# Kernel tuning notes

Measured on AMD Instinct MI355X. Metric: run time of the kernel, lower is better.

The kernel has to match this reference:

```python
import jax, jax.numpy as jnp
import numpy as np

N = 100000
E = 3200000
F_IN = 128
HID = 64
NUM_GRAPHS = 512
NUM_CLASSES = 2


def setup_inputs() -> dict:
    key = jax.random.key(0)
    ks = jax.random.split(key, 8)
    x = jax.random.normal(ks[0], (N, F_IN), dtype=jnp.float32)
    edge_index = jax.random.randint(ks[1], (2, E), 0, N, dtype=jnp.int64)
    batch = jnp.sort(jax.random.randint(ks[2], (N,), 0, NUM_GRAPHS, dtype=jnp.int64))
    # Glorot-style init for GCN weights, PyTorch default-style for fc
    W1 = jax.random.normal(ks[3], (F_IN, HID), dtype=jnp.float32) * (1.0 / np.sqrt(F_IN))
    b1 = jnp.zeros((HID,), dtype=jnp.float32)
    W2 = jax.random.normal(ks[4], (HID, HID), dtype=jnp.float32) * (1.0 / np.sqrt(HID))
    b2 = jnp.zeros((HID,), dtype=jnp.float32)
    Wfc = jax.random.normal(ks[5], (HID, NUM_CLASSES), dtype=jnp.float32) * (1.0 / np.sqrt(HID))
    bfc = jax.random.normal(ks[6], (NUM_CLASSES,), dtype=jnp.float32) * 0.01
    return {"x": x, "edge_index": edge_index, "batch": batch,
            "W1": W1, "b1": b1, "W2": W2, "b2": b2, "Wfc": Wfc, "bfc": bfc}


def _gcn_conv(x, row, col, deg_inv_sqrt, W, b):
    """PyG GCNConv: out[col] += d^{-1/2}[row] d^{-1/2}[col] * (x W)[row], self-loops included in row/col."""
    h = x @ W  # [N, out_dim]
    norm = deg_inv_sqrt[row] * deg_inv_sqrt[col]  # [E+N]
    msgs = h[row] * norm[:, None]  # gather + scale
    out = jax.ops.segment_sum(msgs, col, num_segments=N)  # scatter-add
    return out + b


def reference(x, edge_index, batch, W1, b1, W2, b2, Wfc, bfc):
    # add self-loops once (shared normalization for both layers)
    loop = jnp.arange(N, dtype=edge_index.dtype)
    row = jnp.concatenate([edge_index[0], loop])  # sources
    col = jnp.concatenate([edge_index[1], loop])  # targets
    deg = jax.ops.segment_sum(jnp.ones_like(col, dtype=x.dtype), col, num_segments=N)
    deg_inv_sqrt = jnp.where(deg > 0, jax.lax.rsqrt(deg), 0.0)

    h = jax.nn.relu(_gcn_conv(x, row, col, deg_inv_sqrt, W1, b1))
    h = jax.nn.relu(_gcn_conv(h, row, col, deg_inv_sqrt, W2, b2))

    # global_mean_pool over batch ids
    sums = jax.ops.segment_sum(h, batch, num_segments=NUM_GRAPHS)  # [G, HID]
    counts = jax.ops.segment_sum(jnp.ones((N,), dtype=h.dtype), batch, num_segments=NUM_GRAPHS)
    pooled = sums / jnp.maximum(counts, 1.0)[:, None]

    # dropout p=0.5 is identity in eval mode
    return pooled @ Wfc + bfc  # [G, NUM_CLASSES]
```

## Files before the change

### kernel.cpp

```cpp
#include <hip/hip_runtime.h>

#define N_NODES   100000
#define N_EDGES   3200000
#define F_INP     128
#define HID       64
#define N_GRAPHS  512
#define N_CLASSES 2
#define NB        782
#define SCAT_BLOCKS 256
#define CHUNK     (N_EDGES / SCAT_BLOCKS)

__device__ __forceinline__ unsigned short f2bf(float f) {
    unsigned int u = __float_as_uint(f);
    return (unsigned short)((u + 0x7FFFu + ((u >> 16) & 1u)) >> 16);
}
__device__ __forceinline__ float bf_lo(unsigned int u) { return __uint_as_float(u << 16); }
__device__ __forceinline__ float bf_hi(unsigned int u) { return __uint_as_float(u & 0xFFFF0000u); }

__global__ __launch_bounds__(256) void hist_kernel(const int* __restrict__ ei,
                                                   int* __restrict__ bcnt,
                                                   int* __restrict__ bh) {
    __shared__ int hist[NB];
    for (int i = threadIdx.x; i < NB; i += 256) hist[i] = 0;
    __syncthreads();
    const int e0 = blockIdx.x * CHUNK, e1 = e0 + CHUNK;
    for (int e = e0 + threadIdx.x; e < e1; e += 256)
        atomicAdd(&hist[ei[N_EDGES + e] >> 7], 1);
    __syncthreads();
    for (int i = threadIdx.x; i < NB; i += 256) {
        int v = hist[i];
        bh[(size_t)blockIdx.x * NB + i] = v;
        if (v) atomicAdd(&bcnt[i], v);
    }
}

__global__ __launch_bounds__(1024) void scan_kernel(const int* __restrict__ bcnt,
                                                    int* __restrict__ boff) {
    __shared__ int s[1024];
    const int tid = threadIdx.x;
    const int v = (tid < NB) ? bcnt[tid] : 0;
    s[tid] = v;
    __syncthreads();
    for (int d = 1; d < 1024; d <<= 1) {
        int t = (tid >= d) ? s[tid - d] : 0;
        __syncthreads();
        s[tid] += t;
        __syncthreads();
    }
    if (tid <= NB) boff[tid] = s[tid] - v;
}

__global__ __launch_bounds__(256) void bbase_kernel(int* __restrict__ bh,
                                                    const int* __restrict__ boff) {
    __shared__ int s[256];
    const int b = blockIdx.x;
    const int tid = threadIdx.x;
    const int v = bh[(size_t)tid * NB + b];
    s[tid] = v;
    __syncthreads();
    for (int d = 1; d < 256; d <<= 1) {
        int t = (tid >= d) ? s[tid - d] : 0;
        __syncthreads();
        s[tid] += t;
        __syncthreads();
    }
    bh[(size_t)tid * NB + b] = boff[b] + s[tid] - v;
}

__global__ __launch_bounds__(256) void scatter_kernel(const int* __restrict__ ei,
                                                      const int* __restrict__ bh,
                                                      int* __restrict__ pairs) {
    __shared__ int lbase[NB];
    __shared__ int lcur[NB];
    for (int i = threadIdx.x; i < NB; i += 256) {
        lbase[i] = bh[(size_t)blockIdx.x * NB + i];
        lcur[i] = 0;
    }
    __syncthreads();
    const int e0 = blockIdx.x * CHUNK, e1 = e0 + CHUNK;
    for (int e = e0 + threadIdx.x; e < e1; e += 256) {
        int c = ei[N_EDGES + e];
        int r = ei[e];
        int b = c >> 7;
        int off = atomicAdd(&lcur[b], 1);
        pairs[lbase[b] + off] = r | ((c & 127) << 17);
    }
}

__global__ __launch_bounds__(256) void csr_kernel(const int* __restrict__ pairs,
                                                  const int* __restrict__ boff,
                                                  int* __restrict__ adj,
                                                  int* __restrict__ offs,
                                                  float* __restrict__ dis) {
    __shared__ int cnt[128];
    __shared__ int sc[128];
    __shared__ int base[128];
    __shared__ int cur[128];
    const int tid = threadIdx.x;
    const int b = blockIdx.x;
    const int beg = boff[b], end = boff[b + 1];
    if (tid < 128) { cnt[tid] = 0; cur[tid] = 0; }
    __syncthreads();
    for (int e = beg + tid; e < end; e += 256)
        atomicAdd(&cnt[pairs[e] >> 17], 1);
    __syncthreads();
    if (tid < 128) sc[tid] = cnt[tid];
    __syncthreads();
    for (int d = 1; d < 128; d <<= 1) {
        int t = (tid >= d && tid < 128) ? sc[tid - d] : 0;
        __syncthreads();
        if (tid < 128) sc[tid] += t;
        __syncthreads();
    }
    if (tid < 128) base[tid] = beg + sc[tid] - cnt[tid];
    __syncthreads();
    for (int e = beg + tid; e < end; e += 256) {
        int v = pairs[e];
        int lc = v >> 17;
        int o = atomicAdd(&cur[lc], 1);
        adj[base[lc] + o] = v & 131071;
    }
    const int n = (b << 7) + tid;
    if (tid < 128 && n < N_NODES) {
        offs[n] = base[tid];
        dis[n] = rsqrtf((float)cnt[tid] + 1.0f);
    }
    if (b == 0 && tid == 0) offs[N_NODES] = N_EDGES;
}

__global__ void counts_kernel(const int* __restrict__ batch, int* __restrict__ counts) {
    const int g = blockIdx.x * blockDim.x + threadIdx.x;
    if (g >= N_GRAPHS) return;
    int lo = 0, hi = N_NODES;
    while (lo < hi) { int m = (lo + hi) >> 1; if (batch[m] < g) lo = m + 1; else hi = m; }
    const int l0 = lo;
    lo = 0; hi = N_NODES;
    while (lo < hi) { int m = (lo + hi) >> 1; if (batch[m] < g + 1) lo = m + 1; else hi = m; }
    counts[g] = lo - l0;
}

__global__ __launch_bounds__(256) void mm1_kernel(const float* __restrict__ x,
                                                  const float* __restrict__ W1,
                                                  const float* __restrict__ dis,
                                                  unsigned short* __restrict__ p) {
    __shared__ float ws[F_INP * HID];
    for (int i = threadIdx.x; i < F_INP * HID / 4; i += 256)
        ((float4*)ws)[i] = ((const float4*)W1)[i];
    __syncthreads();
    const int tx = threadIdx.x & 15;
    const int ty = threadIdx.x >> 4;
    const int row0 = blockIdx.x * 64 + ty * 4;
    int r[4];
#pragma unroll
    for (int i = 0; i < 4; ++i) r[i] = min(row0 + i, N_NODES - 1);
    float acc[4][4] = {};
#pragma unroll 2
    for (int k = 0; k < F_INP; k += 4) {
        float4 a[4];
#pragma unroll
        for (int i = 0; i < 4; ++i)
            a[i] = *(const float4*)(x + (size_t)r[i] * F_INP + k);
        float4 w0 = *(const float4*)(ws + (k + 0) * HID + tx * 4);
        float4 w1 = *(const float4*)(ws + (k + 1) * HID + tx * 4);
        float4 w2 = *(const float4*)(ws + (k + 2) * HID + tx * 4);
        float4 w3 = *(const float4*)(ws + (k + 3) * HID + tx * 4);
#pragma unroll
        for (int i = 0; i < 4; ++i) {
            acc[i][0] += a[i].x * w0.x + a[i].y * w1.x + a[i].z * w2.x + a[i].w * w3.x;
            acc[i][1] += a[i].x * w0.y + a[i].y * w1.y + a[i].z * w2.y + a[i].w * w3.y;
            acc[i][2] += a[i].x * w0.z + a[i].y * w1.z + a[i].z * w2.z + a[i].w * w3.z;
            acc[i][3] += a[i].x * w0.w + a[i].y * w1.w + a[i].z * w2.w + a[i].w * w3.w;
        }
    }
#pragma unroll
    for (int i = 0; i < 4; ++i) {
        int rr = row0 + i;
        if (rr < N_NODES) {
            float d = dis[rr];
            ushort4 o;
            o.x = f2bf(d * acc[i][0]);
            o.y = f2bf(d * acc[i][1]);
            o.z = f2bf(d * acc[i][2]);
            o.w = f2bf(d * acc[i][3]);
            *(ushort4*)(p + (size_t)rr * HID + tx * 4) = o;
        }
    }
}

__global__ __launch_bounds__(256) void mm2_kernel(const unsigned short* __restrict__ hb,
                                                  const float* __restrict__ W2,
                                                  const float* __restrict__ dis,
                                                  unsigned short* __restrict__ p) {
    __shared__ float ws[HID * HID];
    for (int i = threadIdx.x; i < HID * HID / 4; i += 256)
        ((float4*)ws)[i] = ((const float4*)W2)[i];
    __syncthreads();
    const int tx = threadIdx.x & 15;
    const int ty = threadIdx.x >> 4;
    const int row0 = blockIdx.x * 64 + ty * 4;
    int r[4];
#pragma unroll
    for (int i = 0; i < 4; ++i) r[i] = min(row0 + i, N_NODES - 1);
    float acc[4][4] = {};
#pragma unroll 2
    for (int k = 0; k < HID; k += 8) {
        uint4 a[4];
#pragma unroll
        for (int i = 0; i < 4; ++i)
            a[i] = *(const uint4*)(hb + (size_t)r[i] * HID + k);
        float4 w[8];
#pragma unroll
        for (int m = 0; m < 8; ++m)
            w[m] = *(const float4*)(ws + (k + m) * HID + tx * 4);
#pragma unroll
        for (int i = 0; i < 4; ++i) {
            float h0 = bf_lo(a[i].x), h1 = bf_hi(a[i].x);
            float h2 = bf_lo(a[i].y), h3 = bf_hi(a[i].y);
            float h4 = bf_lo(a[i].z), h5 = bf_hi(a[i].z);
            float h6 = bf_lo(a[i].w), h7 = bf_hi(a[i].w);
            acc[i][0] += h0 * w[0].x + h1 * w[1].x + h2 * w[2].x + h3 * w[3].x
                       + h4 * w[4].x + h5 * w[5].x + h6 * w[6].x + h7 * w[7].x;
            acc[i][1] += h0 * w[0].y + h1 * w[1].y + h2 * w[2].y + h3 * w[3].y
                       + h4 * w[4].y + h5 * w[5].y + h6 * w[6].y + h7 * w[7].y;
            acc[i][2] += h0 * w[0].z + h1 * w[1].z + h2 * w[2].z + h3 * w[3].z
                       + h4 * w[4].z + h5 * w[5].z + h6 * w[6].z + h7 * w[7].z;
            acc[i][3] += h0 * w[0].w + h1 * w[1].w + h2 * w[2].w + h3 * w[3].w
                       + h4 * w[4].w + h5 * w[5].w + h6 * w[6].w + h7 * w[7].w;
        }
    }
#pragma unroll
    for (int i = 0; i < 4; ++i) {
        int rr = row0 + i;
        if (rr < N_NODES) {
            float d = dis[rr];
            ushort4 o;
            o.x = f2bf(d * acc[i][0]);
            o.y = f2bf(d * acc[i][1]);
            o.z = f2bf(d * acc[i][2]);
            o.w = f2bf(d * acc[i][3]);
            *(ushort4*)(p + (size_t)rr * HID + tx * 4) = o;
        }
    }
}

__device__ __forceinline__ float gather_node(const unsigned short* __restrict__ p,
                                             const int* __restrict__ adj,
                                             int c, int beg, int end, int q, int g) {
    float acc[8];
    {
        uint4 s = *(const uint4*)(p + (size_t)c * HID + g * 8);
        float sm = (q == 0) ? 1.f : 0.f;
        acc[0] = sm * bf_lo(s.x); acc[1] = sm * bf_hi(s.x);
        acc[2] = sm * bf_lo(s.y); acc[3] = sm * bf_hi(s.y);
        acc[4] = sm * bf_lo(s.z); acc[5] = sm * bf_hi(s.z);
        acc[6] = sm * bf_lo(s.w); acc[7] = sm * bf_hi(s.w);
    }
    int e = beg;
    for (; e + 32 <= end; e += 32) {
        int r0 = adj[e + q];
        int r1 = adj[e + 8 + q];
        int r2 = adj[e + 16 + q];
        int r3 = adj[e + 24 + q];
        uint4 v0 = *(const uint4*)(p + (size_t)r0 * HID + g * 8);
        uint4 v1 = *(const uint4*)(p + (size_t)r1 * HID + g * 8);
        uint4 v2 = *(const uint4*)(p + (size_t)r2 * HID + g * 8);
        uint4 v3 = *(const uint4*)(p + (size_t)r3 * HID + g * 8);
        acc[0] += (bf_lo(v0.x) + bf_lo(v1.x)) + (bf_lo(v2.x) + bf_lo(v3.x));
        acc[1] += (bf_hi(v0.x) + bf_hi(v1.x)) + (bf_hi(v2.x) + bf_hi(v3.x));
        acc[2] += (bf_lo(v0.y) + bf_lo(v1.y)) + (bf_lo(v2.y) + bf_lo(v3.y));
        acc[3] += (bf_hi(v0.y) + bf_hi(v1.y)) + (bf_hi(v2.y) + bf_hi(v3.y));
        acc[4] += (bf_lo(v0.z) + bf_lo(v1.z)) + (bf_lo(v2.z) + bf_lo(v3.z));
        acc[5] += (bf_hi(v0.z) + bf_hi(v1.z)) + (bf_hi(v2.z) + bf_hi(v3.z));
        acc[6] += (bf_lo(v0.w) + bf_lo(v1.w)) + (bf_lo(v2.w) + bf_lo(v3.w));
        acc[7] += (bf_hi(v0.w) + bf_hi(v1.w)) + (bf_hi(v2.w) + bf_hi(v3.w));
    }
    for (; e + 16 <= end; e += 16) {
        int r0 = adj[e + q];
        int r1 = adj[e + 8 + q];
        uint4 v0 = *(const uint4*)(p + (size_t)r0 * HID + g * 8);
        uint4 v1 = *(const uint4*)(p + (size_t)r1 * HID + g * 8);
        acc[0] += bf_lo(v0.x) + bf_lo(v1.x); acc[1] += bf_hi(v0.x) + bf_hi(v1.x);
        acc[2] += bf_lo(v0.y) + bf_lo(v1.y); acc[3] += bf_hi(v0.y) + bf_hi(v1.y);
        acc[4] += bf_lo(v0.z) + bf_lo(v1.z); acc[5] += bf_hi(v0.z) + bf_hi(v1.z);
        acc[6] += bf_lo(v0.w) + bf_lo(v1.w); acc[7] += bf_hi(v0.w) + bf_hi(v1.w);
    }
    for (; e < end; e += 8) {
        int idx = e + q;
        int r = adj[min(idx, end - 1)];
        float m = (idx < end) ? 1.f : 0.f;
        uint4 v = *(const uint4*)(p + (size_t)r * HID + g * 8);
        acc[0] = fmaf(m, bf_lo(v.x), acc[0]); acc[1] = fmaf(m, bf_hi(v.x), acc[1]);
        acc[2] = fmaf(m, bf_lo(v.y), acc[2]); acc[3] = fmaf(m, bf_hi(v.y), acc[3]);
        acc[4] = fmaf(m, bf_lo(v.z), acc[4]); acc[5] = fmaf(m, bf_hi(v.z), acc[5]);
        acc[6] = fmaf(m, bf_lo(v.w), acc[6]); acc[7] = fmaf(m, bf_hi(v.w), acc[7]);
    }
#pragma unroll
    for (int j = 0; j < 8; ++j) {
        acc[j] += __shfl_xor(acc[j], 8, 64);
        acc[j] += __shfl_xor(acc[j], 16, 64);
        acc[j] += __shfl_xor(acc[j], 32, 64);
    }
    return (q & 4) ? ((q & 2) ? ((q & 1) ? acc[7] : acc[6]) : ((q & 1) ? acc[5] : acc[4]))
                   : ((q & 2) ? ((q & 1) ? acc[3] : acc[2]) : ((q & 1) ? acc[1] : acc[0]));
}

__global__ __launch_bounds__(256) void gather1_kernel(const unsigned short* __restrict__ p,
                                                      const int* __restrict__ adj,
                                                      const int* __restrict__ offs,
                                                      const float* __restrict__ dis,
                                                      const float* __restrict__ b1,
                                                      unsigned short* __restrict__ hb) {
    const int lane = threadIdx.x & 63;
    const int q = lane >> 3, g = lane & 7;
    const int gwave = (blockIdx.x * blockDim.x + threadIdx.x) >> 6;
    const int nwaves = (gridDim.x * blockDim.x) >> 6;
    const float bj = b1[g * 8 + q];
    for (int c = gwave; c < N_NODES; c += nwaves) {
        const int beg = offs[c], end = offs[c + 1];
        float val = gather_node(p, adj, c, beg, end, q, g);
        hb[(size_t)c * HID + g * 8 + q] = f2bf(fmaxf(dis[c] * val + bj, 0.f));
    }
}

__global__ __launch_bounds__(256) void gather2_kernel(const unsigned short* __restrict__ p,
                                                      const int* __restrict__ adj,
                                                      const int* __restrict__ offs,
                                                      const float* __restrict__ dis,
                                                      const float* __restrict__ b2,
                                                      const int* __restrict__ batch,
                                                      float* __restrict__ sums) {
    const int lane = threadIdx.x & 63;
    const int q = lane >> 3, g = lane & 7;
    const int gwave = (blockIdx.x * blockDim.x + threadIdx.x) >> 6;
    const int nwaves = (gridDim.x * blockDim.x) >> 6;
    const float bj = b2[g * 8 + q];
    for (int c = gwave; c < N_NODES; c += nwaves) {
        const int beg = offs[c], end = offs[c + 1];
        float val = gather_node(p, adj, c, beg, end, q, g);
        float v = fmaxf(dis[c] * val + bj, 0.f);
        atomicAdd(&sums[(size_t)batch[c] * HID + g * 8 + q], v);
    }
}

__global__ void fc_kernel(const float* __restrict__ sums, const int* __restrict__ counts,
                          const float* __restrict__ Wfc, const float* __restrict__ bfc,
                          float* __restrict__ out) {
    const int g = blockIdx.x;
    const int j = threadIdx.x;
    float cnt = fmaxf((float)counts[g], 1.0f);
    float pj = sums[(size_t)g * HID + j] / cnt;
    float a0 = pj * Wfc[j * N_CLASSES + 0];
    float a1 = pj * Wfc[j * N_CLASSES + 1];
    for (int off = 32; off > 0; off >>= 1) {
        a0 += __shfl_down(a0, off, 64);
        a1 += __shfl_down(a1, off, 64);
    }
    if (j == 0) {
        out[g * N_CLASSES + 0] = a0 + bfc[0];
        out[g * N_CLASSES + 1] = a1 + bfc[1];
    }
}

extern "C" void kernel_launch(void* const* d_in, const int* in_sizes, int n_in,
                              void* d_out, int out_size, void* d_ws, size_t ws_size,
                              hipStream_t stream) {
    const float* x     = (const float*)d_in[0];
    const int*   ei    = (const int*)d_in[1];
    const int*   batch = (const int*)d_in[2];
    const float* W1    = (const float*)d_in[3];
    const float* b1    = (const float*)d_in[4];
    const float* W2    = (const float*)d_in[5];
    const float* b2    = (const float*)d_in[6];
    const float* Wfc   = (const float*)d_in[7];
    const float* bfc   = (const float*)d_in[8];
    float* out = (float*)d_out;

    char* ws = (char*)d_ws;
    size_t off = 0;
    auto alloc = [&](size_t bytes) -> void* {
        void* pp = ws + off;
        off += (bytes + 255) & ~(size_t)255;
        return pp;
    };
    int*   bcnt   = (int*)alloc((size_t)NB * 4);
    int*   boff   = (int*)alloc((size_t)(NB + 1) * 4);
    int*   bh     = (int*)alloc((size_t)SCAT_BLOCKS * NB * 4);
    float* dis    = (float*)alloc((size_t)N_NODES * 4);
    int*   pairs  = (int*)alloc((size_t)N_EDGES * 4);
    int*   adj    = (int*)alloc((size_t)N_EDGES * 4);
    int*   offs   = (int*)alloc((size_t)(N_NODES + 1) * 4);
    unsigned short* p  = (unsigned short*)alloc((size_t)N_NODES * HID * 2);
    unsigned short* hb = (unsigned short*)alloc((size_t)N_NODES * HID * 2);
    float* sums   = (float*)alloc((size_t)N_GRAPHS * HID * 4);
    int*   counts = (int*)alloc((size_t)N_GRAPHS * 4);

    hipMemsetAsync(bcnt, 0, (size_t)NB * 4, stream);
    hipMemsetAsync(sums, 0, (size_t)N_GRAPHS * HID * 4, stream);

    hist_kernel<<<SCAT_BLOCKS, 256, 0, stream>>>(ei, bcnt, bh);
    scan_kernel<<<1, 1024, 0, stream>>>(bcnt, boff);
    bbase_kernel<<<NB, 256, 0, stream>>>(bh, boff);
    scatter_kernel<<<SCAT_BLOCKS, 256, 0, stream>>>(ei, bh, pairs);
    csr_kernel<<<NB, 256, 0, stream>>>(pairs, boff, adj, offs, dis);
    counts_kernel<<<2, 256, 0, stream>>>(batch, counts);
    mm1_kernel<<<(N_NODES + 63) / 64, 256, 0, stream>>>(x, W1, dis, p);
    gather1_kernel<<<2048, 256, 0, stream>>>(p, adj, offs, dis, b1, hb);
    mm2_kernel<<<(N_NODES + 63) / 64, 256, 0, stream>>>(hb, W2, dis, p);
    gather2_kernel<<<2048, 256, 0, stream>>>(p, adj, offs, dis, b2, batch, sums);
    fc_kernel<<<N_GRAPHS, 64, 0, stream>>>(sums, counts, Wfc, bfc, out);
}
```

Before: 388.0 us.

## Stage GEMM tiles in LDS, segment-reduce pooling atomics, simplify prefix and reductions

Several independent changes. The per-bucket base computation becomes a serial per-thread scan in a small kernel. Both dense GEMMs first stage their 64-row input tile into shared memory with coalesced loads. The gather reduction uses a butterfly transpose-reduce with fewer shuffles. The gather loops switch to contiguous node ranges per wave so gather2 can accumulate per-graph partial sums and issue far fewer atomics. Graph counts move into the fc kernel via binary search, removing one launch. Extra shared memory in mm1 (64KB) may lower occupancy.

```diff
diff --git a/kernel.cpp b/kernel.cpp
--- a/kernel.cpp
+++ b/kernel.cpp
@@ -50,21 +50,18 @@
     if (tid <= NB) boff[tid] = s[tid] - v;
 }
 
-__global__ __launch_bounds__(256) void bbase_kernel(int* __restrict__ bh,
-                                                    const int* __restrict__ boff) {
-    __shared__ int s[256];
-    const int b = blockIdx.x;
-    const int tid = threadIdx.x;
-    const int v = bh[(size_t)tid * NB + b];
-    s[tid] = v;
-    __syncthreads();
-    for (int d = 1; d < 256; d <<= 1) {
-        int t = (tid >= d) ? s[tid - d] : 0;
-        __syncthreads();
-        s[tid] += t;
-        __syncthreads();
-    }
-    bh[(size_t)tid * NB + b] = boff[b] + s[tid] - v;
+__global__ __launch_bounds__(64) void bbase_kernel(int* __restrict__ bh,
+                                                   const int* __restrict__ boff) {
+    const int b = blockIdx.x * 64 + threadIdx.x;
+    if (b >= NB) return;
+    int base = boff[b];
+    for (int i = 0; i < SCAT_BLOCKS; i += 8) {
+        int v[8];
+#pragma unroll
+        for (int j = 0; j < 8; ++j) v[j] = bh[(size_t)(i + j) * NB + b];
+#pragma unroll
+        for (int j = 0; j < 8; ++j) { bh[(size_t)(i + j) * NB + b] = base; base += v[j]; }
+    }
 }
 
 __global__ __launch_bounds__(256) void scatter_kernel(const int* __restrict__ ei,
@@ -128,38 +125,32 @@
     if (b == 0 && tid == 0) offs[N_NODES] = N_EDGES;
 }
 
-__global__ void counts_kernel(const int* __restrict__ batch, int* __restrict__ counts) {
-    const int g = blockIdx.x * blockDim.x + threadIdx.x;
-    if (g >= N_GRAPHS) return;
-    int lo = 0, hi = N_NODES;
-    while (lo < hi) { int m = (lo + hi) >> 1; if (batch[m] < g) lo = m + 1; else hi = m; }
-    const int l0 = lo;
-    lo = 0; hi = N_NODES;
-    while (lo < hi) { int m = (lo + hi) >> 1; if (batch[m] < g + 1) lo = m + 1; else hi = m; }
-    counts[g] = lo - l0;
-}
-
 __global__ __launch_bounds__(256) void mm1_kernel(const float* __restrict__ x,
                                                   const float* __restrict__ W1,
                                                   const float* __restrict__ dis,
                                                   unsigned short* __restrict__ p) {
+    __shared__ float xs[64 * F_INP];
     __shared__ float ws[F_INP * HID];
     for (int i = threadIdx.x; i < F_INP * HID / 4; i += 256)
         ((float4*)ws)[i] = ((const float4*)W1)[i];
+    const long base4 = (long)blockIdx.x * (64 * F_INP / 4);
+    const long tot4 = (long)N_NODES * F_INP / 4;
+    for (int i = threadIdx.x; i < 64 * F_INP / 4; i += 256) {
+        float4 v = make_float4(0.f, 0.f, 0.f, 0.f);
+        if (base4 + i < tot4) v = ((const float4*)x)[base4 + i];
+        ((float4*)xs)[i] = v;
+    }
     __syncthreads();
     const int tx = threadIdx.x & 15;
     const int ty = threadIdx.x >> 4;
     const int row0 = blockIdx.x * 64 + ty * 4;
-    int r[4];
-#pragma unroll
-    for (int i = 0; i < 4; ++i) r[i] = min(row0 + i, N_NODES - 1);
     float acc[4][4] = {};
-#pragma unroll 2
+#pragma unroll 4
     for (int k = 0; k < F_INP; k += 4) {
         float4 a[4];
 #pragma unroll
         for (int i = 0; i < 4; ++i)
-            a[i] = *(const float4*)(x + (size_t)r[i] * F_INP + k);
+            a[i] = *(const float4*)(xs + (ty * 4 + i) * F_INP + k);
         float4 w0 = *(const float4*)(ws + (k + 0) * HID + tx * 4);
         float4 w1 = *(const float4*)(ws + (k + 1) * HID + tx * 4);
         float4 w2 = *(const float4*)(ws + (k + 2) * HID + tx * 4);
@@ -191,23 +182,28 @@
                                                   const float* __restrict__ W2,
                                                   const float* __restrict__ dis,
                                                   unsigned short* __restrict__ p) {
+    __shared__ unsigned short hs[64 * HID];
     __shared__ float ws[HID * HID];
     for (int i = threadIdx.x; i < HID * HID / 4; i += 256)
         ((float4*)ws)[i] = ((const float4*)W2)[i];
+    const long base8 = (long)blockIdx.x * (64 * HID / 8);
+    const long tot8 = (long)N_NODES * HID / 8;
+    for (int i = threadIdx.x; i < 64 * HID / 8; i += 256) {
+        uint4 v = make_uint4(0u, 0u, 0u, 0u);
+        if (base8 + i < tot8) v = ((const uint4*)hb)[base8 + i];
+        ((uint4*)hs)[i] = v;
+    }
     __syncthreads();
     const int tx = threadIdx.x & 15;
     const int ty = threadIdx.x >> 4;
     const int row0 = blockIdx.x * 64 + ty * 4;
-    int r[4];
-#pragma unroll
-    for (int i = 0; i < 4; ++i) r[i] = min(row0 + i, N_NODES - 1);
     float acc[4][4] = {};
 #pragma unroll 2
     for (int k = 0; k < HID; k += 8) {
         uint4 a[4];
 #pragma unroll
         for (int i = 0; i < 4; ++i)
-            a[i] = *(const uint4*)(hb + (size_t)r[i] * HID + k);
+            a[i] = *(const uint4*)(hs + (ty * 4 + i) * HID + k);
         float4 w[8];
 #pragma unroll
         for (int m = 0; m < 8; ++m)
@@ -294,14 +290,14 @@
         acc[4] = fmaf(m, bf_lo(v.z), acc[4]); acc[5] = fmaf(m, bf_hi(v.z), acc[5]);
         acc[6] = fmaf(m, bf_lo(v.w), acc[6]); acc[7] = fmaf(m, bf_hi(v.w), acc[7]);
     }
-#pragma unroll
-    for (int j = 0; j < 8; ++j) {
-        acc[j] += __shfl_xor(acc[j], 8, 64);
-        acc[j] += __shfl_xor(acc[j], 16, 64);
-        acc[j] += __shfl_xor(acc[j], 32, 64);
-    }
-    return (q & 4) ? ((q & 2) ? ((q & 1) ? acc[7] : acc[6]) : ((q & 1) ? acc[5] : acc[4]))
-                   : ((q & 2) ? ((q & 1) ? acc[3] : acc[2]) : ((q & 1) ? acc[1] : acc[0]));
+    const bool q0 = (q & 1) != 0, q1 = (q & 2) != 0, q2 = (q & 4) != 0;
+    float b0 = (q0 ? acc[1] : acc[0]) + __shfl_xor(q0 ? acc[0] : acc[1], 8, 64);
+    float b1 = (q0 ? acc[3] : acc[2]) + __shfl_xor(q0 ? acc[2] : acc[3], 8, 64);
+    float b2 = (q0 ? acc[5] : acc[4]) + __shfl_xor(q0 ? acc[4] : acc[5], 8, 64);
+    float b3 = (q0 ? acc[7] : acc[6]) + __shfl_xor(q0 ? acc[6] : acc[7], 8, 64);
+    float c0 = (q1 ? b1 : b0) + __shfl_xor(q1 ? b0 : b1, 16, 64);
+    float c1 = (q1 ? b3 : b2) + __shfl_xor(q1 ? b2 : b3, 16, 64);
+    return (q2 ? c1 : c0) + __shfl_xor(q2 ? c0 : c1, 32, 64);
 }
 
 __global__ __launch_bounds__(256) void gather1_kernel(const unsigned short* __restrict__ p,
@@ -314,8 +310,11 @@
     const int q = lane >> 3, g = lane & 7;
     const int gwave = (blockIdx.x * blockDim.x + threadIdx.x) >> 6;
     const int nwaves = (gridDim.x * blockDim.x) >> 6;
+    const int per = (N_NODES + nwaves - 1) / nwaves;
+    const int c0 = gwave * per;
+    const int c1 = min(N_NODES, c0 + per);
     const float bj = b1[g * 8 + q];
-    for (int c = gwave; c < N_NODES; c += nwaves) {
+    for (int c = c0; c < c1; ++c) {
         const int beg = offs[c], end = offs[c + 1];
         float val = gather_node(p, adj, c, beg, end, q, g);
         hb[(size_t)c * HID + g * 8 + q] = f2bf(fmaxf(dis[c] * val + bj, 0.f));
@@ -333,21 +332,39 @@
     const int q = lane >> 3, g = lane & 7;
     const int gwave = (blockIdx.x * blockDim.x + threadIdx.x) >> 6;
     const int nwaves = (gridDim.x * blockDim.x) >> 6;
+    const int per = (N_NODES + nwaves - 1) / nwaves;
+    const int c0 = gwave * per;
+    const int c1 = min(N_NODES, c0 + per);
     const float bj = b2[g * 8 + q];
-    for (int c = gwave; c < N_NODES; c += nwaves) {
+    const int feat = g * 8 + q;
+    float part = 0.f;
+    int gc = -1;
+    for (int c = c0; c < c1; ++c) {
         const int beg = offs[c], end = offs[c + 1];
         float val = gather_node(p, adj, c, beg, end, q, g);
         float v = fmaxf(dis[c] * val + bj, 0.f);
-        atomicAdd(&sums[(size_t)batch[c] * HID + g * 8 + q], v);
-    }
-}
-
-__global__ void fc_kernel(const float* __restrict__ sums, const int* __restrict__ counts,
+        int gid = batch[c];
+        if (gid != gc) {
+            if (gc >= 0) atomicAdd(&sums[(size_t)gc * HID + feat], part);
+            part = 0.f;
+            gc = gid;
+        }
+        part += v;
+    }
+    if (gc >= 0) atomicAdd(&sums[(size_t)gc * HID + feat], part);
+}
+
+__global__ void fc_kernel(const float* __restrict__ sums, const int* __restrict__ batch,
                           const float* __restrict__ Wfc, const float* __restrict__ bfc,
                           float* __restrict__ out) {
     const int g = blockIdx.x;
     const int j = threadIdx.x;
-    float cnt = fmaxf((float)counts[g], 1.0f);
+    int lo = 0, hi = N_NODES;
+    while (lo < hi) { int m = (lo + hi) >> 1; if (batch[m] < g) lo = m + 1; else hi = m; }
+    const int l0 = lo;
+    lo = 0; hi = N_NODES;
+    while (lo < hi) { int m = (lo + hi) >> 1; if (batch[m] < g + 1) lo = m + 1; else hi = m; }
+    float cnt = fmaxf((float)(lo - l0), 1.0f);
     float pj = sums[(size_t)g * HID + j] / cnt;
     float a0 = pj * Wfc[j * N_CLASSES + 0];
     float a1 = pj * Wfc[j * N_CLASSES + 1];
@@ -392,20 +409,18 @@
     unsigned short* p  = (unsigned short*)alloc((size_t)N_NODES * HID * 2);
     unsigned short* hb = (unsigned short*)alloc((size_t)N_NODES * HID * 2);
     float* sums   = (float*)alloc((size_t)N_GRAPHS * HID * 4);
-    int*   counts = (int*)alloc((size_t)N_GRAPHS * 4);
 
     hipMemsetAsync(bcnt, 0, (size_t)NB * 4, stream);
     hipMemsetAsync(sums, 0, (size_t)N_GRAPHS * HID * 4, stream);
 
     hist_kernel<<<SCAT_BLOCKS, 256, 0, stream>>>(ei, bcnt, bh);
     scan_kernel<<<1, 1024, 0, stream>>>(bcnt, boff);
-    bbase_kernel<<<NB, 256, 0, stream>>>(bh, boff);
+    bbase_kernel<<<(NB + 63) / 64, 64, 0, stream>>>(bh, boff);
     scatter_kernel<<<SCAT_BLOCKS, 256, 0, stream>>>(ei, bh, pairs);
     csr_kernel<<<NB, 256, 0, stream>>>(pairs, boff, adj, offs, dis);
-    counts_kernel<<<2, 256, 0, stream>>>(batch, counts);
     mm1_kernel<<<(N_NODES + 63) / 64, 256, 0, stream>>>(x, W1, dis, p);
     gather1_kernel<<<2048, 256, 0, stream>>>(p, adj, offs, dis, b1, hb);
     mm2_kernel<<<(N_NODES + 63) / 64, 256, 0, stream>>>(hb, W2, dis, p);
     gather2_kernel<<<2048, 256, 0, stream>>>(p, adj, offs, dis, b2, batch, sums);
-    fc_kernel<<<N_GRAPHS, 64, 0, stream>>>(sums, counts, Wfc, bfc, out);
-}
+    fc_kernel<<<N_GRAPHS, 64, 0, stream>>>(sums, batch, Wfc, bfc, out);
+}
```

Result: faster. 360.3 us (-7.1%).
